# Optimization experiments

Hardware: AMD Instinct MI355X
Metric: run time of the kernel (lower is better)

The kernel has to match this reference:

```python
import jax, jax.numpy as jnp
import numpy as np

B, S, E, H = 4, 2048, 1024, 16
D = E // H  # head_dim = 64
ROPE_BASE = 10000.0


def _rope(x):
    # x: [B, H, S, D] -> rotary position embedding applied over seq dim
    seq_len = x.shape[2]
    inv_freq = 1.0 / (ROPE_BASE ** (jnp.arange(0, D, 2, dtype=jnp.float32) / D))  # [D/2]
    freqs = jnp.arange(seq_len, dtype=jnp.float32)[:, None] * inv_freq[None, :]   # [S, D/2]
    emb = jnp.concatenate([freqs, freqs], axis=-1)                                 # [S, D]
    cos = jnp.cos(emb).astype(x.dtype)
    sin = jnp.sin(emb).astype(x.dtype)
    x1, x2 = jnp.split(x, 2, axis=-1)
    rotated = jnp.concatenate([-x2, x1], axis=-1)
    return x * cos + rotated * sin


def setup_inputs() -> dict:
    key = jax.random.key(0)
    ks = jax.random.split(key, 10)
    p = 0.02
    return {
        "x": jax.random.normal(ks[0], (B, S, E), dtype=jnp.float32),
        "Wq": jax.random.normal(ks[1], (E, E), dtype=jnp.float32) * p,
        "bq": jnp.zeros((E,), dtype=jnp.float32),
        "Wk": jax.random.normal(ks[2], (E, E), dtype=jnp.float32) * p,
        "bk": jnp.zeros((E,), dtype=jnp.float32),
        "Wv": jax.random.normal(ks[3], (E, E), dtype=jnp.float32) * p,
        "bv": jnp.zeros((E,), dtype=jnp.float32),
        "Wo": jax.random.normal(ks[4], (E, E), dtype=jnp.float32) * p,
        "bo": jnp.zeros((E,), dtype=jnp.float32),
        "key_padding_mask": jnp.zeros((B, S), dtype=bool),
    }


def reference(x, Wq, bq, Wk, bk, Wv, bv, Wo, bo, key_padding_mask):
    b, s, _ = x.shape
    # QKV projections -> [B, H, S, D]
    def proj(W, bias):
        return (x @ W + bias).reshape(b, s, H, D).transpose(0, 2, 1, 3)
    q = _rope(proj(Wq, bq))
    k = _rope(proj(Wk, bk))
    v = proj(Wv, bv)
    scale = D ** -0.5
    scores = jnp.einsum('bhqd,bhkd->bhqk', q, k) * scale  # [B, H, S, S]
    scores = jnp.where(key_padding_mask[:, None, None, :], jnp.finfo(scores.dtype).min, scores)
    probs = jax.nn.softmax(scores, axis=-1)
    out = jnp.einsum('bhqk,bhkd->bhqd', probs, v)         # [B, H, S, D]
    out = out.transpose(0, 2, 1, 3).reshape(b, s, E)
    return out @ Wo + bo
```

## Files before the change

### kernel.cpp

```cpp
#include <hip/hip_runtime.h>
#include <hip/hip_bf16.h>
#include <math.h>

#define Bn 4
#define Sn 2048
#define En 1024
#define Hn 16
#define Dn 64
#define Mn (Bn * Sn)

typedef __attribute__((ext_vector_type(8))) short short8;
typedef __attribute__((ext_vector_type(4))) short short4v;
typedef __attribute__((ext_vector_type(4))) float f32x4;
typedef __attribute__((ext_vector_type(16))) float f32x16;
typedef __attribute__((ext_vector_type(2))) unsigned int uint2v;

#if __has_builtin(__builtin_amdgcn_exp2f)
#define EXP2(x) __builtin_amdgcn_exp2f(x)
#else
#define EXP2(x) exp2f(x)
#endif

#if __has_builtin(__builtin_amdgcn_permlane32_swap)
#define HAVE_PLSWAP 1
#endif

#define GLOAD16(g, s) __builtin_amdgcn_global_load_lds( \
    (const __attribute__((address_space(1))) unsigned int*)(g), \
    (__attribute__((address_space(3))) unsigned int*)(s), 16, 0, 0)

__device__ inline unsigned short f2bf(float f) {
    unsigned int u = __float_as_uint(f);
    u += 0x7FFFu + ((u >> 16) & 1u);
    return (unsigned short)(u >> 16);
}
__device__ inline float bf2f(unsigned short h) {
    return __uint_as_float(((unsigned int)h) << 16);
}
__device__ inline short8 ld8s(const unsigned short* p) {
    union { short4v h[2]; short8 v; } r;
    r.h[0] = *(const short4v*)p;
    r.h[1] = *(const short4v*)(p + 4);
    return r.v;
}
__device__ inline short8 g8(const unsigned short* p) {
    union { int4 i; short8 v; } r;
    r.i = *(const int4*)p;
    return r.v;
}

__device__ inline void st16(unsigned short* base, int row, int col16, int4 v) {
    const unsigned off = ((unsigned)(row * 128 + col16 * 2)) ^ ((unsigned)((row & 7) << 4));
    *(int4*)((char*)base + off) = v;
}
__device__ inline short8 ld16(const unsigned short* base, int row, int col16) {
    const unsigned off = ((unsigned)(row * 128 + col16 * 2)) ^ ((unsigned)((row & 7) << 4));
    union { int4 i; short8 v; } r;
    r.i = *(const int4*)((const char*)base + off);
    return r.v;
}

__global__ __launch_bounds__(256) void convx_kernel(
    const float* __restrict__ X, unsigned short* __restrict__ Xh) {
    int i = blockIdx.x * 256 + threadIdx.x;
    float4 v = ((const float4*)X)[i];
    float f[4] = {v.x, v.y, v.z, v.w};
    short4v h;
#pragma unroll
    for (int j = 0; j < 4; ++j) h[j] = (short)f2bf(f[j]);
    ((short4v*)Xh)[i] = h;
}

__global__ __launch_bounds__(256) void tconv5_kernel(
    const float* __restrict__ Wq, const float* __restrict__ Wk,
    const float* __restrict__ Wv, const float* __restrict__ Wo,
    unsigned short* __restrict__ WqkvT, unsigned short* __restrict__ WoT,
    float* __restrict__ ct, float* __restrict__ st) {
    const int m = blockIdx.z;
    if (m == 4) {
        const int i = (blockIdx.y * 16 + blockIdx.x) * 256 + threadIdx.x;
        const int s = i >> 5, p = i & 31;
        double inv = pow(10000.0, -(double)p / 32.0);
        double a = (double)s * inv;
        ct[i] = (float)cos(a);
        st[i] = (float)sin(a);
        return;
    }
    const float* W = (m == 0) ? Wq : (m == 1) ? Wk : (m == 2) ? Wv : Wo;
    unsigned short* dst = (m < 3) ? WqkvT + (size_t)m * En * En : WoT;

    __shared__ float Ws[64][65];
    const int t = threadIdx.x;
    const int kb = blockIdx.y * 64, nb = blockIdx.x * 64;
    const int lr = t >> 2, lc = (t & 3) * 16;
#pragma unroll
    for (int u = 0; u < 4; ++u) {
        float4 v = *(const float4*)&W[(size_t)(kb + lr) * En + nb + lc + 4 * u];
        Ws[lr][lc + 4 * u + 0] = v.x; Ws[lr][lc + 4 * u + 1] = v.y;
        Ws[lr][lc + 4 * u + 2] = v.z; Ws[lr][lc + 4 * u + 3] = v.w;
    }
    __syncthreads();
    const int orow = t >> 2, ock = (t & 3) * 16;
#pragma unroll
    for (int u = 0; u < 4; ++u) {
        short4v hs;
#pragma unroll
        for (int j = 0; j < 4; ++j) hs[j] = (short)f2bf(Ws[ock + 4 * u + j][orow]);
        *(short4v*)&dst[(size_t)(nb + orow) * En + kb + ock + 4 * u] = hs;
    }
}

template <int KN, int EPI>
__global__ __launch_bounds__(256, 4) void gemm97(
    const unsigned short* __restrict__ A, const unsigned short* __restrict__ Bt,
    const float* __restrict__ b0, const float* __restrict__ bkv,
    const float* __restrict__ bvv,
    unsigned short* __restrict__ oQ, unsigned short* __restrict__ oK,
    unsigned short* __restrict__ oV, float* __restrict__ oF,
    const float* __restrict__ ct, const float* __restrict__ st) {
    __shared__ __align__(16) unsigned short shmem[17408];
    unsigned short (*As)[64] = (unsigned short(*)[64])&shmem[0];
    unsigned short (*Bs)[64] = (unsigned short(*)[64])&shmem[8192];
    const int t = threadIdx.x;
    const int w = t >> 6, l = t & 63;
    const int wm = w & 1, wn = w >> 1;
    const int q = l >> 4, ln16 = l & 15;
    const int r8 = l >> 3, i8 = l & 7;

    int bx = blockIdx.x, by = blockIdx.y;
    {
        const int gx = gridDim.x;
        const int nwg = gx * gridDim.y;
        if ((nwg & 7) == 0) {
            const int n = by * gx + bx;
            const int s = (n & 7) * (nwg >> 3) + (n >> 3);
            bx = s % gx; by = s / gx;
        }
    }
    const int m0 = by * 128, n0 = bx * 128;

    f32x4 acc[4][4];
#pragma unroll
    for (int i = 0; i < 4; ++i)
#pragma unroll
        for (int j = 0; j < 4; ++j)
#pragma unroll
            for (int r = 0; r < 4; ++r) acc[i][j][r] = 0.0f;

    const unsigned short* Ag = &A[(size_t)(m0 + 32 * w + r8) * KN + 8 * i8];
    const unsigned short* Bg = &Bt[(size_t)(n0 + 32 * w + r8) * KN + 8 * i8];

    for (int k0 = 0; k0 < KN; k0 += 64) {
        __syncthreads();
#pragma unroll
        for (int j = 0; j < 4; ++j) {
            GLOAD16(Ag + (size_t)(8 * j) * KN + k0, &As[32 * w + 8 * j][0]);
            GLOAD16(Bg + (size_t)(8 * j) * KN + k0, &Bs[32 * w + 8 * j][0]);
        }
        __syncthreads();
#pragma unroll
        for (int ks = 0; ks < 2; ++ks) {
            short8 af[4], bf[4];
#pragma unroll
            for (int i = 0; i < 4; ++i)
                af[i] = ld8s(&As[64 * wm + 16 * i + ln16][32 * ks + 8 * q]);
#pragma unroll
            for (int j = 0; j < 4; ++j)
                bf[j] = ld8s(&Bs[64 * wn + 16 * j + ln16][32 * ks + 8 * q]);
#pragma unroll
            for (int i = 0; i < 4; ++i)
#pragma unroll
                for (int j = 0; j < 4; ++j)
                    acc[i][j] = __builtin_amdgcn_mfma_f32_16x16x32_bf16(
                        af[i], bf[j], acc[i][j], 0, 0, 0);
        }
    }

    if (EPI == 0) {
#pragma unroll
        for (int i = 0; i < 4; ++i)
#pragma unroll
            for (int r = 0; r < 4; ++r) {
                const int m = m0 + 64 * wm + 16 * i + 4 * q + r;
#pragma unroll
                for (int j = 0; j < 4; ++j) {
                    const int n = n0 + 64 * wn + 16 * j + ln16;
                    oF[(size_t)m * En + n] = acc[i][j][r] + b0[n];
                }
            }
    } else {
        const int mat = n0 >> 10;
        const int nIn0 = n0 & 1023;
        if (mat == 2) {
            __syncthreads();
#pragma unroll
            for (int i = 0; i < 4; ++i)
#pragma unroll
                for (int j = 0; j < 4; ++j) {
                    const int dl = 64 * wn + 16 * j + ln16;
                    const float bv2 = bvv[nIn0 + dl];
#pragma unroll
                    for (int r = 0; r < 4; ++r) {
                        const int sl = 64 * wm + 16 * i + 4 * q + r;
                        shmem[dl * 136 + sl] = f2bf(acc[i][j][r] + bv2);
                    }
                }
            __syncthreads();
            const int dr2 = t >> 1, sc2 = (t & 1) * 64;
            const int hh2 = (nIn0 >> 6) + (dr2 >> 6);
            unsigned short* vp =
                &oV[(((size_t)((m0 >> 11) * Hn + hh2)) * Dn + (dr2 & 63)) * Sn
                    + (m0 & (Sn - 1)) + sc2];
            const unsigned short* tp = &shmem[dr2 * 136 + sc2];
#pragma unroll
            for (int u = 0; u < 8; ++u)
                *(int4*)(vp + 8 * u) = *(const int4*)(tp + 8 * u);
        } else {
            const int nIn = nIn0 + 64 * wn;
            const int hh = nIn >> 6;
            const float* bias = (mat == 0) ? b0 : bkv;
            unsigned short* op = (mat == 0) ? oQ : oK;
#pragma unroll
            for (int i = 0; i < 4; ++i)
#pragma unroll
                for (int r = 0; r < 4; ++r) {
                    const int m = m0 + 64 * wm + 16 * i + 4 * q + r;
                    const int b = m >> 11, s2 = m & (Sn - 1);
                    const size_t base = (((size_t)(b * Hn + hh)) * Sn + s2) * Dn;
#pragma unroll
                    for (int j = 0; j < 2; ++j) {
                        const int nh = 16 * j + ln16;
                        float v0 = acc[i][j][r] + bias[nIn + nh];
                        float v1 = acc[i][j + 2][r] + bias[nIn + nh + 32];
                        float c = ct[s2 * 32 + nh], sn = st[s2 * 32 + nh];
                        float o0 = v0 * c - v1 * sn;
                        float o1 = v1 * c + v0 * sn;
                        if (mat == 0) {
                            o0 *= 0.18033688011112042f;
                            o1 *= 0.18033688011112042f;
                        }
                        op[base + nh] = f2bf(o0);
                        op[base + nh + 32] = f2bf(o1);
                    }
                }
        }
    }
}

__device__ inline void softpack(const f32x16& accS, unsigned long long bm,
                                int c, int h2, float* lsum, unsigned* pw) {
#pragma unroll
    for (int g = 0; g < 4; ++g)
#pragma unroll
        for (int j = 0; j < 2; ++j) {
            const int r0 = 4 * g + 2 * j;
            float p0 = EXP2(accS[r0]);
            float p1 = EXP2(accS[r0 + 1]);
            if (bm) {
                const int key = 32 * c + 8 * g + 4 * h2 + 2 * j;
                if ((bm >> key) & 1) p0 = 0.0f;
                if ((bm >> (key + 1)) & 1) p1 = 0.0f;
            }
            const unsigned u0 = __float_as_uint(p0) & 0xFFFF0000u;
            const unsigned u1 = __float_as_uint(p1) & 0xFFFF0000u;
            lsum[g] += __uint_as_float(u0);
            lsum[g] += __uint_as_float(u1);
            pw[2 * g + j] = (u0 >> 16) | u1;
        }
}

__device__ inline short8 pv_afrag(const unsigned* pw, int s, int h2) {
    union { unsigned u[4]; short8 v; } af;
#ifdef HAVE_PLSWAP
    uint2v r02 = __builtin_amdgcn_permlane32_swap(
        pw[4 * s + 0], pw[4 * s + 2], false, false);
    uint2v r13 = __builtin_amdgcn_permlane32_swap(
        pw[4 * s + 1], pw[4 * s + 3], false, false);
    af.u[0] = r02[0]; af.u[1] = r13[0];
    af.u[2] = r02[1]; af.u[3] = r13[1];
#else
    const unsigned x0 = pw[4 * s + 0], x1 = pw[4 * s + 1];
    const unsigned y0 = pw[4 * s + 2], y1 = pw[4 * s + 3];
    const unsigned py0 = (unsigned)__shfl_xor((int)y0, 32);
    const unsigned py1 = (unsigned)__shfl_xor((int)y1, 32);
    const unsigned px0 = (unsigned)__shfl_xor((int)x0, 32);
    const unsigned px1 = (unsigned)__shfl_xor((int)x1, 32);
    af.u[0] = h2 ? py0 : x0;
    af.u[1] = h2 ? py1 : x1;
    af.u[2] = h2 ? y0 : px0;
    af.u[3] = h2 ? y1 : px1;
#endif
    return af.v;
}

__global__ __launch_bounds__(256) void attn_mfma_kernel(
    const unsigned short* __restrict__ Qb, const unsigned short* __restrict__ Kb,
    const unsigned short* __restrict__ VbT, const unsigned char* __restrict__ mask,
    unsigned short* __restrict__ Obuf) {
    __shared__ __align__(16) unsigned short Ks[2][64][64];
    __shared__ __align__(16) unsigned short Vs[2][64][64];

    const int t = threadIdx.x;
    const int w = t >> 6, l = t & 63, h2 = l >> 5, ln = l & 31;
    const int q0 = blockIdx.x * 128;
    const int h = blockIdx.y, b = blockIdx.z;
    const size_t ho = ((size_t)(b * Hn + h)) * Sn * Dn;
    const unsigned char* maskB = mask + (size_t)b * Sn;

    short8 qh[4];
    const int qrow = q0 + 32 * w + ln;
#pragma unroll
    for (int s = 0; s < 4; ++s)
        qh[s] = g8(&Qb[ho + (size_t)qrow * Dn + 16 * s + 8 * h2]);

    f32x16 accO0, accO1;
#pragma unroll
    for (int i = 0; i < 16; ++i) { accO0[i] = 0.0f; accO1[i] = 0.0f; }
    float lsum[4] = {0.0f, 0.0f, 0.0f, 0.0f};

    const int kr = t >> 2, kc = (t & 3) * 16;
    const unsigned short* Kp = &Kb[ho + (size_t)kr * Dn + kc];
    const unsigned short* Vp = &VbT[ho + (size_t)kr * Sn + kc];

    int4 ck0 = *(const int4*)Kp, ck1 = *(const int4*)(Kp + 8);
    int4 cv0 = *(const int4*)Vp, cv1 = *(const int4*)(Vp + 8);
    unsigned char cm = maskB[l];

#pragma unroll 2
    for (int kt = 0; kt < Sn / 64; ++kt) {
        const int pb = kt & 1;
        unsigned short* KsP = &Ks[pb][0][0];
        unsigned short* VsP = &Vs[pb][0][0];
        st16(KsP, kr, kc, ck0); st16(KsP, kr, kc + 8, ck1);
        st16(VsP, kr, kc, cv0); st16(VsP, kr, kc + 8, cv1);
        const unsigned long long bm = __ballot(cm != 0);
        __syncthreads();
        const int kn = ((kt + 1) & (Sn / 64 - 1)) * 64;
        ck0 = *(const int4*)(Kp + (size_t)kn * Dn);
        ck1 = *(const int4*)(Kp + (size_t)kn * Dn + 8);
        cv0 = *(const int4*)(Vp + kn);
        cv1 = *(const int4*)(Vp + kn + 8);
        cm = maskB[kn + l];

#pragma unroll
        for (int c = 0; c < 2; ++c) {
            short8 kf[4];
#pragma unroll
            for (int s = 0; s < 4; ++s)
                kf[s] = ld16(KsP, 32 * c + ln, 16 * s + 8 * h2);
            f32x16 accS;
#pragma unroll
            for (int i = 0; i < 16; ++i) accS[i] = 0.0f;
            __builtin_amdgcn_s_setprio(1);
#pragma unroll
            for (int s = 0; s < 4; ++s)
                accS = __builtin_amdgcn_mfma_f32_32x32x16_bf16(kf[s], qh[s], accS, 0, 0, 0);
            __builtin_amdgcn_s_setprio(0);

            unsigned pw[8];
            softpack(accS, bm, c, h2, lsum, pw);

#pragma unroll
            for (int s = 0; s < 2; ++s) {
                short8 af = pv_afrag(pw, s, h2);
                short8 vA = ld16(VsP, ln, 32 * c + 16 * s + 8 * h2);
                short8 vB = ld16(VsP, 32 + ln, 32 * c + 16 * s + 8 * h2);
                __builtin_amdgcn_s_setprio(1);
                accO0 = __builtin_amdgcn_mfma_f32_32x32x16_bf16(af, vA, accO0, 0, 0, 0);
                accO1 = __builtin_amdgcn_mfma_f32_32x32x16_bf16(af, vB, accO1, 0, 0, 0);
                __builtin_amdgcn_s_setprio(0);
            }
        }
    }

    const float lme = (lsum[0] + lsum[1]) + (lsum[2] + lsum[3]);
    const float tot = lme + __shfl_xor(lme, 32);
    const float linv = 1.0f / fmaxf(tot, 1e-37f);
#pragma unroll
    for (int r = 0; r < 16; ++r) {
        const int row = (r & 3) + 8 * (r >> 2) + 4 * h2;
        const float lr = __shfl(linv, row);
        const int s = q0 + 32 * w + row;
        const size_t base = ((size_t)b * Sn + s) * 1024 + h * Dn;
        Obuf[base + ln] = f2bf(accO0[r] * lr);
        Obuf[base + 32 + ln] = f2bf(accO1[r] * lr);
    }
}

extern "C" void kernel_launch(void* const* d_in, const int* in_sizes, int n_in,
                              void* d_out, int out_size, void* d_ws, size_t ws_size,
                              hipStream_t stream) {
    const float* x  = (const float*)d_in[0];
    const float* Wq = (const float*)d_in[1];
    const float* bq = (const float*)d_in[2];
    const float* Wk = (const float*)d_in[3];
    const float* bk = (const float*)d_in[4];
    const float* Wv = (const float*)d_in[5];
    const float* bv = (const float*)d_in[6];
    const float* Wo = (const float*)d_in[7];
    const float* bo = (const float*)d_in[8];
    const unsigned char* mask = (const unsigned char*)d_in[9];

    const size_t NE = (size_t)Mn * En;
    const size_t WN = (size_t)En * En;
    unsigned short* ws = (unsigned short*)d_ws;
    unsigned short* Xh = ws;
    unsigned short* Qb = Xh + NE;
    unsigned short* Kb = Qb + NE;
    unsigned short* VbT = Kb + NE;
    unsigned short* Obuf = VbT + NE;
    unsigned short* WqkvT = Obuf + NE;
    unsigned short* WoT = WqkvT + 3 * WN;
    float* ct = (float*)(WoT + WN);
    float* st = ct + (size_t)Sn * 32;

    convx_kernel<<<(int)(NE / 1024), 256, 0, stream>>>(x, Xh);
    tconv5_kernel<<<dim3(16, 16, 5), 256, 0, stream>>>(
        Wq, Wk, Wv, Wo, WqkvT, WoT, ct, st);

    gemm97<En, 1><<<dim3(3 * En / 128, Mn / 128), 256, 0, stream>>>(
        Xh, WqkvT, bq, bk, bv, Qb, Kb, VbT, nullptr, ct, st);

    attn_mfma_kernel<<<dim3(Sn / 128, Hn, Bn), 256, 0, stream>>>(
        Qb, Kb, VbT, mask, Obuf);

    gemm97<En, 0><<<dim3(En / 128, Mn / 128), 256, 0, stream>>>(
        Obuf, WoT, bo, nullptr, nullptr, nullptr, nullptr, nullptr,
        (float*)d_out, ct, st);
}
```

Before: 305.7 us.

## Merge prep kernels into one launch and add smaller-tile output projection GEMM

The separate x-to-bf16 conversion kernel and the weight transpose/RoPE-table kernel are merged into one prep launch, with extra z-slices handling the x conversion. This removes a kernel launch and lets the two prep jobs overlap. The output projection now uses a new 64x128-tile, 128-thread GEMM instead of the 128x128 gemm97 path, which doubles the block count (8x128 = 1024 blocks) for better CU occupancy on the small N=1024 GEMM. The new GEMM has no double buffering and loads more B data per unit of A reuse, so its memory efficiency per tile is lower.

```diff
diff --git a/kernel.cpp b/kernel.cpp
--- a/kernel.cpp
+++ b/kernel.cpp
@@ -60,25 +60,26 @@
     return r.v;
 }
 
-__global__ __launch_bounds__(256) void convx_kernel(
-    const float* __restrict__ X, unsigned short* __restrict__ Xh) {
-    int i = blockIdx.x * 256 + threadIdx.x;
-    float4 v = ((const float4*)X)[i];
-    float f[4] = {v.x, v.y, v.z, v.w};
-    short4v h;
-#pragma unroll
-    for (int j = 0; j < 4; ++j) h[j] = (short)f2bf(f[j]);
-    ((short4v*)Xh)[i] = h;
-}
-
-__global__ __launch_bounds__(256) void tconv5_kernel(
+__global__ __launch_bounds__(256) void prep_kernel(
+    const float* __restrict__ X, unsigned short* __restrict__ Xh,
     const float* __restrict__ Wq, const float* __restrict__ Wk,
     const float* __restrict__ Wv, const float* __restrict__ Wo,
     unsigned short* __restrict__ WqkvT, unsigned short* __restrict__ WoT,
     float* __restrict__ ct, float* __restrict__ st) {
     const int m = blockIdx.z;
+    const int t = threadIdx.x;
+    if (m >= 5) {
+        const int i = ((m - 5) * 256 + blockIdx.y * 16 + blockIdx.x) * 256 + t;
+        float4 v = ((const float4*)X)[i];
+        float f[4] = {v.x, v.y, v.z, v.w};
+        short4v h;
+#pragma unroll
+        for (int j = 0; j < 4; ++j) h[j] = (short)f2bf(f[j]);
+        ((short4v*)Xh)[i] = h;
+        return;
+    }
     if (m == 4) {
-        const int i = (blockIdx.y * 16 + blockIdx.x) * 256 + threadIdx.x;
+        const int i = (blockIdx.y * 16 + blockIdx.x) * 256 + t;
         const int s = i >> 5, p = i & 31;
         double inv = pow(10000.0, -(double)p / 32.0);
         double a = (double)s * inv;
@@ -90,7 +91,6 @@
     unsigned short* dst = (m < 3) ? WqkvT + (size_t)m * En * En : WoT;
 
     __shared__ float Ws[64][65];
-    const int t = threadIdx.x;
     const int kb = blockIdx.y * 64, nb = blockIdx.x * 64;
     const int lr = t >> 2, lc = (t & 3) * 16;
 #pragma unroll
@@ -110,13 +110,13 @@
     }
 }
 
-template <int KN, int EPI>
+template <int KN>
 __global__ __launch_bounds__(256, 4) void gemm97(
     const unsigned short* __restrict__ A, const unsigned short* __restrict__ Bt,
     const float* __restrict__ b0, const float* __restrict__ bkv,
     const float* __restrict__ bvv,
     unsigned short* __restrict__ oQ, unsigned short* __restrict__ oK,
-    unsigned short* __restrict__ oV, float* __restrict__ oF,
+    unsigned short* __restrict__ oV,
     const float* __restrict__ ct, const float* __restrict__ st) {
     __shared__ __align__(16) unsigned short shmem[17408];
     unsigned short (*As)[64] = (unsigned short(*)[64])&shmem[0];
@@ -176,75 +176,132 @@
         }
     }
 
-    if (EPI == 0) {
+    const int mat = n0 >> 10;
+    const int nIn0 = n0 & 1023;
+    if (mat == 2) {
+        __syncthreads();
+#pragma unroll
+        for (int i = 0; i < 4; ++i)
+#pragma unroll
+            for (int j = 0; j < 4; ++j) {
+                const int dl = 64 * wn + 16 * j + ln16;
+                const float bv2 = bvv[nIn0 + dl];
+#pragma unroll
+                for (int r = 0; r < 4; ++r) {
+                    const int sl = 64 * wm + 16 * i + 4 * q + r;
+                    shmem[dl * 136 + sl] = f2bf(acc[i][j][r] + bv2);
+                }
+            }
+        __syncthreads();
+        const int dr2 = t >> 1, sc2 = (t & 1) * 64;
+        const int hh2 = (nIn0 >> 6) + (dr2 >> 6);
+        unsigned short* vp =
+            &oV[(((size_t)((m0 >> 11) * Hn + hh2)) * Dn + (dr2 & 63)) * Sn
+                + (m0 & (Sn - 1)) + sc2];
+        const unsigned short* tp = &shmem[dr2 * 136 + sc2];
+#pragma unroll
+        for (int u = 0; u < 8; ++u)
+            *(int4*)(vp + 8 * u) = *(const int4*)(tp + 8 * u);
+    } else {
+        const int nIn = nIn0 + 64 * wn;
+        const int hh = nIn >> 6;
+        const float* bias = (mat == 0) ? b0 : bkv;
+        unsigned short* op = (mat == 0) ? oQ : oK;
 #pragma unroll
         for (int i = 0; i < 4; ++i)
 #pragma unroll
             for (int r = 0; r < 4; ++r) {
                 const int m = m0 + 64 * wm + 16 * i + 4 * q + r;
-#pragma unroll
-                for (int j = 0; j < 4; ++j) {
-                    const int n = n0 + 64 * wn + 16 * j + ln16;
-                    oF[(size_t)m * En + n] = acc[i][j][r] + b0[n];
+                const int b = m >> 11, s2 = m & (Sn - 1);
+                const size_t base = (((size_t)(b * Hn + hh)) * Sn + s2) * Dn;
+#pragma unroll
+                for (int j = 0; j < 2; ++j) {
+                    const int nh = 16 * j + ln16;
+                    float v0 = acc[i][j][r] + bias[nIn + nh];
+                    float v1 = acc[i][j + 2][r] + bias[nIn + nh + 32];
+                    float c = ct[s2 * 32 + nh], sn = st[s2 * 32 + nh];
+                    float o0 = v0 * c - v1 * sn;
+                    float o1 = v1 * c + v0 * sn;
+                    if (mat == 0) {
+                        o0 *= 0.18033688011112042f;
+                        o1 *= 0.18033688011112042f;
+                    }
+                    op[base + nh] = f2bf(o0);
+                    op[base + nh + 32] = f2bf(o1);
                 }
             }
-    } else {
-        const int mat = n0 >> 10;
-        const int nIn0 = n0 & 1023;
-        if (mat == 2) {
-            __syncthreads();
+    }
+}
+
+__global__ __launch_bounds__(128, 4) void gemm64o(
+    const unsigned short* __restrict__ A, const unsigned short* __restrict__ Bt,
+    const float* __restrict__ b0, float* __restrict__ oF) {
+    __shared__ unsigned short As[64][64];
+    __shared__ unsigned short Bs[128][64];
+    const int t = threadIdx.x;
+    const int w = t >> 6, l = t & 63;
+    const int q = l >> 4, ln16 = l & 15;
+    const int r8 = l >> 3, i8 = l & 7;
+
+    int bx = blockIdx.x, by = blockIdx.y;
+    {
+        const int gx = gridDim.x;
+        const int nwg = gx * gridDim.y;
+        const int n = by * gx + bx;
+        const int s = (n & 7) * (nwg >> 3) + (n >> 3);
+        bx = s % gx; by = s / gx;
+    }
+    const int m0 = by * 64, n0 = bx * 128;
+
+    f32x4 acc[4][4];
+#pragma unroll
+    for (int i = 0; i < 4; ++i)
+#pragma unroll
+        for (int j = 0; j < 4; ++j)
+#pragma unroll
+            for (int r = 0; r < 4; ++r) acc[i][j][r] = 0.0f;
+
+    const unsigned short* Ag = &A[(size_t)(m0 + 32 * w + r8) * En + 8 * i8];
+    const unsigned short* Bg = &Bt[(size_t)(n0 + 64 * w + r8) * En + 8 * i8];
+
+    for (int k0 = 0; k0 < En; k0 += 64) {
+        __syncthreads();
+#pragma unroll
+        for (int j = 0; j < 4; ++j)
+            GLOAD16(Ag + (size_t)(8 * j) * En + k0, &As[32 * w + 8 * j][0]);
+#pragma unroll
+        for (int j = 0; j < 8; ++j)
+            GLOAD16(Bg + (size_t)(8 * j) * En + k0, &Bs[64 * w + 8 * j][0]);
+        __syncthreads();
+#pragma unroll
+        for (int ks = 0; ks < 2; ++ks) {
+            short8 af[4], bf[4];
 #pragma unroll
             for (int i = 0; i < 4; ++i)
-#pragma unroll
-                for (int j = 0; j < 4; ++j) {
-                    const int dl = 64 * wn + 16 * j + ln16;
-                    const float bv2 = bvv[nIn0 + dl];
-#pragma unroll
-                    for (int r = 0; r < 4; ++r) {
-                        const int sl = 64 * wm + 16 * i + 4 * q + r;
-                        shmem[dl * 136 + sl] = f2bf(acc[i][j][r] + bv2);
-                    }
-                }
-            __syncthreads();
-            const int dr2 = t >> 1, sc2 = (t & 1) * 64;
-            const int hh2 = (nIn0 >> 6) + (dr2 >> 6);
-            unsigned short* vp =
-                &oV[(((size_t)((m0 >> 11) * Hn + hh2)) * Dn + (dr2 & 63)) * Sn
-                    + (m0 & (Sn - 1)) + sc2];
-            const unsigned short* tp = &shmem[dr2 * 136 + sc2];
-#pragma unroll
-            for (int u = 0; u < 8; ++u)
-                *(int4*)(vp + 8 * u) = *(const int4*)(tp + 8 * u);
-        } else {
-            const int nIn = nIn0 + 64 * wn;
-            const int hh = nIn >> 6;
-            const float* bias = (mat == 0) ? b0 : bkv;
-            unsigned short* op = (mat == 0) ? oQ : oK;
+                af[i] = ld8s(&As[16 * i + ln16][32 * ks + 8 * q]);
+#pragma unroll
+            for (int j = 0; j < 4; ++j)
+                bf[j] = ld8s(&Bs[64 * w + 16 * j + ln16][32 * ks + 8 * q]);
 #pragma unroll
             for (int i = 0; i < 4; ++i)
 #pragma unroll
-                for (int r = 0; r < 4; ++r) {
-                    const int m = m0 + 64 * wm + 16 * i + 4 * q + r;
-                    const int b = m >> 11, s2 = m & (Sn - 1);
-                    const size_t base = (((size_t)(b * Hn + hh)) * Sn + s2) * Dn;
-#pragma unroll
-                    for (int j = 0; j < 2; ++j) {
-                        const int nh = 16 * j + ln16;
-                        float v0 = acc[i][j][r] + bias[nIn + nh];
-                        float v1 = acc[i][j + 2][r] + bias[nIn + nh + 32];
-                        float c = ct[s2 * 32 + nh], sn = st[s2 * 32 + nh];
-                        float o0 = v0 * c - v1 * sn;
-                        float o1 = v1 * c + v0 * sn;
-                        if (mat == 0) {
-                            o0 *= 0.18033688011112042f;
-                            o1 *= 0.18033688011112042f;
-                        }
-                        op[base + nh] = f2bf(o0);
-                        op[base + nh + 32] = f2bf(o1);
-                    }
-                }
-        }
-    }
+                for (int j = 0; j < 4; ++j)
+                    acc[i][j] = __builtin_amdgcn_mfma_f32_16x16x32_bf16(
+                        af[i], bf[j], acc[i][j], 0, 0, 0);
+        }
+    }
+
+#pragma unroll
+    for (int i = 0; i < 4; ++i)
+#pragma unroll
+        for (int r = 0; r < 4; ++r) {
+            const int m = m0 + 16 * i + 4 * q + r;
+#pragma unroll
+            for (int j = 0; j < 4; ++j) {
+                const int n = n0 + 64 * w + 16 * j + ln16;
+                oF[(size_t)m * En + n] = acc[i][j][r] + b0[n];
+            }
+        }
 }
 
 __device__ inline void softpack(const f32x16& accS, unsigned long long bm,
@@ -414,17 +471,15 @@
     float* ct = (float*)(WoT + WN);
     float* st = ct + (size_t)Sn * 32;
 
-    convx_kernel<<<(int)(NE / 1024), 256, 0, stream>>>(x, Xh);
-    tconv5_kernel<<<dim3(16, 16, 5), 256, 0, stream>>>(
-        Wq, Wk, Wv, Wo, WqkvT, WoT, ct, st);
-
-    gemm97<En, 1><<<dim3(3 * En / 128, Mn / 128), 256, 0, stream>>>(
-        Xh, WqkvT, bq, bk, bv, Qb, Kb, VbT, nullptr, ct, st);
+    prep_kernel<<<dim3(16, 16, 37), 256, 0, stream>>>(
+        x, Xh, Wq, Wk, Wv, Wo, WqkvT, WoT, ct, st);
+
+    gemm97<En><<<dim3(3 * En / 128, Mn / 128), 256, 0, stream>>>(
+        Xh, WqkvT, bq, bk, bv, Qb, Kb, VbT, ct, st);
 
     attn_mfma_kernel<<<dim3(Sn / 128, Hn, Bn), 256, 0, stream>>>(
         Qb, Kb, VbT, mask, Obuf);
 
-    gemm97<En, 0><<<dim3(En / 128, Mn / 128), 256, 0, stream>>>(
-        Obuf, WoT, bo, nullptr, nullptr, nullptr, nullptr, nullptr,
-        (float*)d_out, ct, st);
-}
+    gemm64o<<<dim3(En / 128, Mn / 64), 128, 0, stream>>>(
+        Obuf, WoT, bo, (float*)d_out);
+}
```

After: 298.6 us. -2.3%, faster.
